# Kernel optimization log

Measured on AMD Instinct MI355X. Metric: run time of the kernel, lower is better.

## Reference

```python
import jax, jax.numpy as jnp
import numpy as np

B, S, H, NH, HD = 2, 2048, 2048, 16, 128
MASK_VALUE = -1e10


def setup_inputs() -> dict:
    key = jax.random.key(0)
    ks = jax.random.split(key, 5)
    scale = 1.0 / np.sqrt(H)
    x = jax.random.normal(ks[0], (B, S, H), dtype=jnp.float32)
    Wq = jax.random.normal(ks[1], (H, NH * HD), dtype=jnp.float32) * scale
    Wk = jax.random.normal(ks[2], (H, NH * HD), dtype=jnp.float32) * scale
    Wv = jax.random.normal(ks[3], (H, NH * HD), dtype=jnp.float32) * scale
    Wo = jax.random.normal(ks[4], (NH * HD, H), dtype=jnp.float32) * scale
    # causal boolean mask (B, S, S) as in decoder-style gemma usage
    mask = jnp.broadcast_to(jnp.tril(jnp.ones((S, S), dtype=bool)), (B, S, S))
    return {"x": x, "mask": mask, "Wq": Wq, "Wk": Wk, "Wv": Wv, "Wo": Wo}


def reference(x, mask, Wq, Wk, Wv, Wo):
    b, s, h = x.shape
    # bias-free QKV projections, split into heads -> (b, nh, s, hd)
    def split_heads(y):
        return y.reshape(b, s, NH, HD).transpose(0, 2, 1, 3)
    q = split_heads(x @ Wq)
    k = split_heads(x @ Wk)
    v = split_heads(x @ Wv)
    scores = jnp.einsum('bhtd,bhTd->bhtT', q, k) / jnp.sqrt(jnp.asarray(HD, x.dtype))
    scores = jnp.where(mask[:, None, :, :], scores, MASK_VALUE)
    weights = jax.nn.softmax(scores, axis=-1)
    out = jnp.einsum('bhtT,bhTd->bhtd', weights, v)
    out = out.transpose(0, 2, 1, 3).reshape(b, s, NH * HD)
    return out @ Wo
```

## Files before the change

kernel.cpp:

```cpp
#include <hip/hip_runtime.h>
#include <hip/hip_bf16.h>
#include <stdint.h>

#define DEVFN __device__ __forceinline__

typedef __attribute__((ext_vector_type(8))) short short8;
typedef __attribute__((ext_vector_type(4))) float f32x4;
typedef __attribute__((ext_vector_type(16))) float f32x16;

constexpr int S_LEN = 2048;
constexpr int HDIM  = 2048;
constexpr int NHEAD = 16;
constexpr int HD    = 128;

DEVFN unsigned short f2bf(float f){
  union { float f; unsigned u; } x; x.f = f;
  unsigned r = x.u + 0x7fffu + ((x.u >> 16) & 1u);
  return (unsigned short)(r >> 16);
}

typedef const __attribute__((address_space(1))) void* gas1_ptr;
typedef __attribute__((address_space(3))) void* las3_ptr;

DEVFN void gl_lds16(const void* g, void* l){
  __builtin_amdgcn_global_load_lds((gas1_ptr)g, (las3_ptr)l, 16, 0, 0);
}

DEVFN f32x4 mfma16(short8 a, short8 b, f32x4 c){
  return __builtin_amdgcn_mfma_f32_16x16x32_bf16(a, b, c, 0, 0, 0);
}

DEVFN f32x16 mfma32(short8 a, short8 b, f32x16 c){
  return __builtin_amdgcn_mfma_f32_32x32x16_bf16(a, b, c, 0, 0, 0);
}

DEVFN unsigned cvtpk_bf16(float lo, float hi){
  unsigned w;
  asm("v_cvt_pk_bf16_f32 %0, %1, %2" : "=v"(w) : "v"(lo), "v"(hi));
  return w;
}


__global__ void cast_x_kernel(const float* __restrict__ in, unsigned short* __restrict__ out){
  int i = (blockIdx.x * 256 + threadIdx.x) * 4;
  float4 v = *(const float4*)(in + i);
  ushort4 o;
  o.x = f2bf(v.x); o.y = f2bf(v.y); o.z = f2bf(v.z); o.w = f2bf(v.w);
  *(ushort4*)(out + i) = o;
}

__global__ void transpose_cast_w(const float* __restrict__ in, unsigned short* __restrict__ out){
  __shared__ float tile[32][33];
  int tx = threadIdx.x, ty = threadIdx.y;
  int kb = blockIdx.x * 32, nb = blockIdx.y * 32;
  #pragma unroll
  for (int i = 0; i < 4; i++)
    tile[ty + i*8][tx] = in[(size_t)(kb + ty + i*8) * HDIM + nb + tx];
  __syncthreads();
  #pragma unroll
  for (int i = 0; i < 4; i++)
    out[(size_t)(nb + ty + i*8) * HDIM + kb + tx] = f2bf(tile[tx][ty + i*8]);
}

__global__ void transpose_v_kernel(const unsigned short* __restrict__ in,
                                   unsigned short* __restrict__ out){
  __shared__ unsigned short tile[32][34];
  int tx = threadIdx.x, ty = threadIdx.y;
  int sb = blockIdx.x * 32, db = blockIdx.y * 32, bh = blockIdx.z;
  const unsigned short* ip = in + (size_t)bh * S_LEN * HD;
  unsigned short* op = out + (size_t)bh * S_LEN * HD;
  #pragma unroll
  for (int i = 0; i < 4; i++)
    tile[ty + i*8][tx] = ip[(size_t)(sb + ty + i*8) * HD + db + tx];
  __syncthreads();
  #pragma unroll
  for (int i = 0; i < 4; i++)
    op[(size_t)(db + ty + i*8) * S_LEN + sb + tx] = tile[tx][ty + i*8];
}


DEVFN void gemm_core_bt(const unsigned short* __restrict__ A,
                        const unsigned short* __restrict__ Bt,
                        int K, int m0, int n0,
                        unsigned short* lsA, unsigned short* lsB,
                        f32x4 (&acc)[4][4]){
  const int t = threadIdx.x;
  const int wid = t >> 6, lane = t & 63;
  const int wr = wid >> 1, wc = wid & 1;
  const int l15 = lane & 15, lg = lane >> 4;

  for (int k0 = 0; k0 < K; k0 += 64){
    __syncthreads();
    #pragma unroll
    for (int i = 0; i < 4; i++){
      int o = (t + i*256) * 16;
      int row = o >> 7;
      int col = (o & 127) ^ ((row & 7) << 4);
      gl_lds16((const char*)A + ((size_t)(m0 + row) * K + k0) * 2 + col, (char*)lsA + o);
    }
    #pragma unroll
    for (int i = 0; i < 4; i++){
      int o = (t + i*256) * 16;
      int row = o >> 7;
      int col = (o & 127) ^ ((row & 7) << 4);
      gl_lds16((const char*)Bt + ((size_t)(n0 + row) * K + k0) * 2 + col, (char*)lsB + o);
    }
    __syncthreads();
    #pragma unroll
    for (int kk = 0; kk < 2; kk++){
      short8 af[4], bfr[4];
      #pragma unroll
      for (int i = 0; i < 4; i++){
        int ra = wr*64 + i*16 + l15;
        af[i]  = *(const short8*)((const char*)lsA + ra*128 + ((kk*64 + lg*16) ^ ((ra & 7) << 4)));
        int rb = wc*64 + i*16 + l15;
        bfr[i] = *(const short8*)((const char*)lsB + rb*128 + ((kk*64 + lg*16) ^ ((rb & 7) << 4)));
      }
      #pragma unroll
      for (int i = 0; i < 4; i++)
        #pragma unroll
        for (int j = 0; j < 4; j++)
          acc[i][j] = mfma16(af[i], bfr[j], acc[i][j]);
    }
  }
}

__global__ __launch_bounds__(256, 2)
void gemm_qkv(const unsigned short* __restrict__ xb, const unsigned short* __restrict__ Wt,
              unsigned short* __restrict__ Qb, unsigned short* __restrict__ Kb,
              unsigned short* __restrict__ Vb){
  __shared__ __align__(16) unsigned short lsA[128*64];
  __shared__ __align__(16) unsigned short lsB[128*64];
  f32x4 acc[4][4];
  const f32x4 z4 = {0.f, 0.f, 0.f, 0.f};
  #pragma unroll
  for (int i = 0; i < 4; i++)
    #pragma unroll
    for (int j = 0; j < 4; j++) acc[i][j] = z4;

  gemm_core_bt(xb, Wt, HDIM, blockIdx.x*128, blockIdx.y*128, lsA, lsB, acc);

  const float qscale = 0.08838834764831845f * 1.4426950408889634f;
  const int t = threadIdx.x, wid = t >> 6, lane = t & 63;
  const int wr = wid >> 1, wc = wid & 1, l15 = lane & 15, lg = lane >> 4;
  #pragma unroll
  for (int j = 0; j < 4; j++){
    int n = blockIdx.y*128 + wc*64 + j*16 + l15;
    int sel = n >> 11, hh = (n >> 7) & 15, d = n & 127;
    unsigned short* base = (sel == 0) ? Qb : ((sel == 1) ? Kb : Vb);
    float sc = (sel == 0) ? qscale : 1.0f;
    #pragma unroll
    for (int i = 0; i < 4; i++){
      #pragma unroll
      for (int r = 0; r < 4; r++){
        int m = blockIdx.x*128 + wr*64 + i*16 + lg*4 + r;
        int bb = m >> 11, ss = m & 2047;
        base[(((size_t)bb * NHEAD + hh) * S_LEN + ss) * HD + d] = f2bf(acc[i][j][r] * sc);
      }
    }
  }
}

__global__ __launch_bounds__(256, 2)
void gemm_out(const unsigned short* __restrict__ Ob, const unsigned short* __restrict__ Wot,
              float* __restrict__ out){
  __shared__ __align__(16) unsigned short lsA[128*64];
  __shared__ __align__(16) unsigned short lsB[128*64];
  f32x4 acc[4][4];
  const f32x4 z4 = {0.f, 0.f, 0.f, 0.f};
  #pragma unroll
  for (int i = 0; i < 4; i++)
    #pragma unroll
    for (int j = 0; j < 4; j++) acc[i][j] = z4;

  gemm_core_bt(Ob, Wot, HDIM, blockIdx.x*128, blockIdx.y*128, lsA, lsB, acc);

  const int t = threadIdx.x, wid = t >> 6, lane = t & 63;
  const int wr = wid >> 1, wc = wid & 1, l15 = lane & 15, lg = lane >> 4;
  #pragma unroll
  for (int i = 0; i < 4; i++){
    #pragma unroll
    for (int r = 0; r < 4; r++){
      int m = blockIdx.x*128 + wr*64 + i*16 + lg*4 + r;
      #pragma unroll
      for (int j = 0; j < 4; j++){
        int n = blockIdx.y*128 + wc*64 + j*16 + l15;
        out[(size_t)m * HDIM + n] = acc[i][j][r];
      }
    }
  }
}

__global__ __launch_bounds__(256, 2)
void attn_kernel(const unsigned short* __restrict__ Q,
                 const unsigned short* __restrict__ Kg,
                 const unsigned short* __restrict__ Vt,
                 unsigned short* __restrict__ Ob){
  __shared__ __align__(16) unsigned short Kl[2][64*128];
  __shared__ __align__(16) unsigned short Vl[2][128*64];

  const int t = threadIdx.x;
  const int wid = t >> 6, lane = t & 63;
  const int l31 = lane & 31, hi = lane >> 5;
  const int L = blockIdx.x;
  const int bh = L & 31;
  const int z = L >> 5;
  const int qt = (z < 8) ? z : 23 - z;
  const int b = bh >> 4, h = bh & 15;
  const unsigned short* Qp = Q  + (size_t)bh * S_LEN * HD;
  const unsigned short* Kp = Kg + (size_t)bh * S_LEN * HD;
  const unsigned short* Vp = Vt + (size_t)bh * S_LEN * HD;
  const int q0 = qt * 128;
  const int wrow0 = q0 + wid * 32;
  const int qrow = wrow0 + l31;
  const int nt = 2 * qt + 2;

  auto stage = [&](int buf, int k0){
    #pragma unroll
    for (int i = 0; i < 4; i++){
      int o = (t + i*256) * 16;
      int row = o >> 8;
      int col = (o & 255) ^ ((row & 15) << 4);
      gl_lds16((const char*)(Kp + (size_t)(k0 + row) * HD) + col, (char*)&Kl[buf][0] + o);
    }
    #pragma unroll
    for (int i = 0; i < 4; i++){
      int o = (t + i*256) * 16;
      int row = o >> 7;
      int col = (o & 127) ^ ((row & 7) << 4);
      gl_lds16((const char*)(Vp + (size_t)row * S_LEN + k0) + col, (char*)&Vl[buf][0] + o);
    }
  };

  short8 qf[8];
  #pragma unroll
  for (int dk = 0; dk < 8; dk++)
    qf[dk] = *(const short8*)(Qp + (size_t)qrow * HD + dk*16 + hi*8);

  f32x16 oacc[4];
  #pragma unroll
  for (int db = 0; db < 4; db++)
    #pragma unroll
    for (int r = 0; r < 16; r++) oacc[db][r] = 0.f;
  float mrun = -1e30f, lsum = 0.f;

  stage(0, 0);
  asm volatile("s_waitcnt vmcnt(0)" ::: "memory");
  __builtin_amdgcn_s_barrier();

  int cur = 0;
  #pragma unroll 1
  for (int tdx = 0; tdx < nt; tdx++){
    if (tdx + 1 < nt) stage(cur ^ 1, (tdx + 1) * 64);
    const int k0 = tdx * 64;

    if (k0 <= wrow0 + 31){
      const char* Kb_ = (const char*)&Kl[cur][0];
      const char* Vb_ = (const char*)&Vl[cur][0];

      f32x16 sacc[2];
      #pragma unroll
      for (int cb = 0; cb < 2; cb++)
        #pragma unroll
        for (int r = 0; r < 16; r++) sacc[cb][r] = 0.f;
      __builtin_amdgcn_s_setprio(1);
      #pragma unroll
      for (int dk = 0; dk < 8; dk++){
        #pragma unroll
        for (int cb = 0; cb < 2; cb++){
          int kr = cb*32 + l31;
          short8 af = *(const short8*)(Kb_ + kr*256 + ((dk*32 + hi*16) ^ ((kr & 15) << 4)));
          sacc[cb] = mfma32(af, qf[dk], sacc[cb]);
        }
      }
      __builtin_amdgcn_s_setprio(0);

      if (k0 + 64 > wrow0){
        #pragma unroll
        for (int cb = 0; cb < 2; cb++)
          #pragma unroll
          for (int r = 0; r < 16; r++){
            int kcol = k0 + cb*32 + (r & 3) + 8*(r >> 2) + 4*hi;
            if (kcol > qrow) sacc[cb][r] = -1e30f;
          }
      }

      float mv[8];
      #pragma unroll
      for (int i = 0; i < 8; i++)
        mv[i] = fmaxf(fmaxf(sacc[0][i], sacc[0][i+8]), fmaxf(sacc[1][i], sacc[1][i+8]));
      #pragma unroll
      for (int s = 4; s > 0; s >>= 1)
        #pragma unroll
        for (int i = 0; i < 4; i++)
          if (i < s) mv[i] = fmaxf(mv[i], mv[i+s]);
      float mx = fmaxf(mv[0], __shfl_xor(mv[0], 32, 64));
      if (!__all(mx <= mrun + 8.f)){
        float mnew = fmaxf(mrun, mx);
        float alpha = exp2f(mrun - mnew);
        mrun = mnew;
        lsum *= alpha;
        #pragma unroll
        for (int db = 0; db < 4; db++)
          #pragma unroll
          for (int r = 0; r < 16; r++) oacc[db][r] *= alpha;
      }
      float ls = 0.f;
      #pragma unroll
      for (int cb = 0; cb < 2; cb++)
        #pragma unroll
        for (int r = 0; r < 16; r++){
          float p = exp2f(sacc[cb][r] - mrun);
          sacc[cb][r] = p;
          ls += p;
        }
      lsum += ls;

      short8 pa[4];
      #pragma unroll
      for (int ks = 0; ks < 4; ks++){
        int cb = ks >> 1, bs = (ks & 1) * 8;
        unsigned A1 = cvtpk_bf16(sacc[cb][bs+4], sacc[cb][bs+5]);
        unsigned B1 = cvtpk_bf16(sacc[cb][bs+0], sacc[cb][bs+1]);
        unsigned A2 = cvtpk_bf16(sacc[cb][bs+6], sacc[cb][bs+7]);
        unsigned B2 = cvtpk_bf16(sacc[cb][bs+2], sacc[cb][bs+3]);
        unsigned oA1 = __shfl_xor(A1, 32, 64), oB1 = __shfl_xor(B1, 32, 64);
        unsigned oA2 = __shfl_xor(A2, 32, 64), oB2 = __shfl_xor(B2, 32, 64);
        union { unsigned u[4]; short8 v; } pk;
        pk.u[0] = hi ? oA1 : B1;
        pk.u[1] = hi ? oA2 : B2;
        pk.u[2] = hi ? A1 : oB1;
        pk.u[3] = hi ? A2 : oB2;
        pa[ks] = pk.v;
      }

      __builtin_amdgcn_s_setprio(1);
      #pragma unroll
      for (int ks = 0; ks < 4; ks++){
        #pragma unroll
        for (int db = 0; db < 4; db++){
          int vr = db*32 + l31;
          short8 vf = *(const short8*)(Vb_ + vr*128 + ((ks*32 + hi*16) ^ ((vr & 7) << 4)));
          oacc[db] = mfma32(vf, pa[ks], oacc[db]);
        }
      }
      __builtin_amdgcn_s_setprio(0);
    }

    asm volatile("s_waitcnt vmcnt(0)" ::: "memory");
    __builtin_amdgcn_s_barrier();
    cur ^= 1;
  }

  float lt = lsum + __shfl_xor(lsum, 32, 64);
  float inv = 1.f / lt;
  #pragma unroll
  for (int db = 0; db < 4; db++)
    #pragma unroll
    for (int r = 0; r < 16; r++) oacc[db][r] *= inv;

  char* reg_lds = (char*)&Kl[0][0] + wid * 8192;
  #pragma unroll
  for (int ms = 0; ms < 8; ms++){
    int db = ms >> 1, bs = (ms & 1) * 8;
    unsigned A1 = cvtpk_bf16(oacc[db][bs+4], oacc[db][bs+5]);
    unsigned B1 = cvtpk_bf16(oacc[db][bs+0], oacc[db][bs+1]);
    unsigned A2 = cvtpk_bf16(oacc[db][bs+6], oacc[db][bs+7]);
    unsigned B2 = cvtpk_bf16(oacc[db][bs+2], oacc[db][bs+3]);
    unsigned oA1 = __shfl_xor(A1, 32, 64), oB1 = __shfl_xor(B1, 32, 64);
    unsigned oA2 = __shfl_xor(A2, 32, 64), oB2 = __shfl_xor(B2, 32, 64);
    union { unsigned u[4]; short8 v; } pk;
    pk.u[0] = hi ? oA1 : B1;
    pk.u[1] = hi ? oA2 : B2;
    pk.u[2] = hi ? A1 : oB1;
    pk.u[3] = hi ? A2 : oB2;
    int byteo = l31*256 + ((ms*32 + hi*16) ^ ((l31 & 7) << 4));
    *(short8*)(reg_lds + byteo) = pk.v;
  }
  #pragma unroll
  for (int i = 0; i < 8; i++){
    int r = (lane >> 4) + i*4;
    int c = lane & 15;
    short8 v = *(const short8*)(reg_lds + r*256 + ((c*16) ^ ((r & 7) << 4)));
    *(short8*)(Ob + ((size_t)(b * S_LEN + wrow0 + r)) * 2048 + h*128 + c*8) = v;
  }
}

extern "C" void kernel_launch(void* const* d_in, const int* in_sizes, int n_in,
                              void* d_out, int out_size, void* d_ws, size_t ws_size,
                              hipStream_t stream){
  const float* x  = (const float*)d_in[0];
  const float* Wq = (const float*)d_in[2];
  const float* Wk = (const float*)d_in[3];
  const float* Wv = (const float*)d_in[4];
  const float* Wo = (const float*)d_in[5];

  char* ws = (char*)d_ws;
  unsigned short* xb  = (unsigned short*)(ws);
  unsigned short* Wt  = (unsigned short*)(ws + 16777216);
  unsigned short* Wot = (unsigned short*)(ws + 41943040);
  unsigned short* Qb  = (unsigned short*)(ws + 50331648);
  unsigned short* Kb  = (unsigned short*)(ws + 67108864);
  unsigned short* Vb  = (unsigned short*)(ws + 83886080);
  unsigned short* Vt  = Wt;
  unsigned short* Ob  = xb;

  dim3 tb(32, 8);
  cast_x_kernel<<<8192, 256, 0, stream>>>(x, xb);
  transpose_cast_w<<<dim3(64, 64), tb, 0, stream>>>(Wq, Wt);
  transpose_cast_w<<<dim3(64, 64), tb, 0, stream>>>(Wk, Wt + 2048*2048);
  transpose_cast_w<<<dim3(64, 64), tb, 0, stream>>>(Wv, Wt + 2*2048*2048);
  transpose_cast_w<<<dim3(64, 64), tb, 0, stream>>>(Wo, Wot);

  gemm_qkv<<<dim3(32, 48), 256, 0, stream>>>(xb, Wt, Qb, Kb, Vb);

  transpose_v_kernel<<<dim3(64, 4, 32), tb, 0, stream>>>(Vb, Vt);

  attn_kernel<<<512, 256, 0, stream>>>(Qb, Kb, Vt, Ob);

  gemm_out<<<dim3(32, 16), 256, 0, stream>>>(Ob, Wot, (float*)d_out);
}
```

Before: 257.4 us.

## Triple-buffer GEMM LDS with 256x128 tiles, swizzled grid, fused weight casts

Both GEMMs are rewritten around a shared core. It uses 512-thread blocks with 256x128 output tiles and a three-stage LDS ring fed by async global-to-LDS loads. Partial `s_waitcnt vmcnt` waits plus a single barrier per k-step let the next two tiles load while the current one computes. A block-index swizzle groups neighbouring tiles for L2 reuse, and the four weight transpose-casts become one launch over a z dimension. The cost is about 144KB of LDS per block, which allows only one block per CU, and this relies on latency hiding coming from the pipeline rather than from occupancy.

Measured after the change: 261.8 us. About the same (+1.7%).

```diff
diff --git a/kernel.cpp b/kernel.cpp
--- a/kernel.cpp
+++ b/kernel.cpp
@@ -49,17 +49,21 @@
   *(ushort4*)(out + i) = o;
 }
 
-__global__ void transpose_cast_w(const float* __restrict__ in, unsigned short* __restrict__ out){
+__global__ void transpose_cast_w4(const float* __restrict__ w0, const float* __restrict__ w1,
+                                  const float* __restrict__ w2, const float* __restrict__ w3,
+                                  unsigned short* __restrict__ out){
   __shared__ float tile[32][33];
   int tx = threadIdx.x, ty = threadIdx.y;
-  int kb = blockIdx.x * 32, nb = blockIdx.y * 32;
+  int kb = blockIdx.x * 32, nb = blockIdx.y * 32, z = blockIdx.z;
+  const float* in = (z == 0) ? w0 : (z == 1) ? w1 : (z == 2) ? w2 : w3;
+  unsigned short* op = out + (size_t)z * HDIM * HDIM;
   #pragma unroll
   for (int i = 0; i < 4; i++)
     tile[ty + i*8][tx] = in[(size_t)(kb + ty + i*8) * HDIM + nb + tx];
   __syncthreads();
   #pragma unroll
   for (int i = 0; i < 4; i++)
-    out[(size_t)(nb + ty + i*8) * HDIM + kb + tx] = f2bf(tile[tx][ty + i*8]);
+    op[(size_t)(nb + ty + i*8) * HDIM + kb + tx] = f2bf(tile[tx][ty + i*8]);
 }
 
 __global__ void transpose_v_kernel(const unsigned short* __restrict__ in,
@@ -78,43 +82,55 @@
     op[(size_t)(db + ty + i*8) * S_LEN + sb + tx] = tile[tx][ty + i*8];
 }
 
-
-DEVFN void gemm_core_bt(const unsigned short* __restrict__ A,
-                        const unsigned short* __restrict__ Bt,
-                        int K, int m0, int n0,
-                        unsigned short* lsA, unsigned short* lsB,
-                        f32x4 (&acc)[4][4]){
-  const int t = threadIdx.x;
-  const int wid = t >> 6, lane = t & 63;
+DEVFN void gemm_core3(const unsigned short* __restrict__ A,
+                      const unsigned short* __restrict__ Bt,
+                      int K, int m0, int n0, char* ls, f32x4 (&acc)[4][4]){
+  const int tid = threadIdx.x;
+  const int wid = tid >> 6, lane = tid & 63;
   const int wr = wid >> 1, wc = wid & 1;
   const int l15 = lane & 15, lg = lane >> 4;
-
-  for (int k0 = 0; k0 < K; k0 += 64){
-    __syncthreads();
+  const int nt = K >> 6;
+
+  auto stage = [&](int buf, int kt){
+    const char* Ab = (const char*)A + (size_t)kt * 128;
+    const char* Bb = (const char*)Bt + (size_t)kt * 128;
+    char* lb = ls + buf * 49152;
     #pragma unroll
     for (int i = 0; i < 4; i++){
-      int o = (t + i*256) * 16;
+      int o = (tid + i*512) * 16;
       int row = o >> 7;
       int col = (o & 127) ^ ((row & 7) << 4);
-      gl_lds16((const char*)A + ((size_t)(m0 + row) * K + k0) * 2 + col, (char*)lsA + o);
-    }
-    #pragma unroll
-    for (int i = 0; i < 4; i++){
-      int o = (t + i*256) * 16;
-      int row = o >> 7;
-      int col = (o & 127) ^ ((row & 7) << 4);
-      gl_lds16((const char*)Bt + ((size_t)(n0 + row) * K + k0) * 2 + col, (char*)lsB + o);
-    }
-    __syncthreads();
+      gl_lds16(Ab + (size_t)(m0 + row) * (K*2) + col, lb + o);
+    }
+    #pragma unroll
+    for (int i = 4; i < 6; i++){
+      int o = (tid + i*512) * 16;
+      int ob = o - 32768;
+      int row = ob >> 7;
+      int col = (ob & 127) ^ ((row & 7) << 4);
+      gl_lds16(Bb + (size_t)(n0 + row) * (K*2) + col, lb + o);
+    }
+  };
+
+  stage(0, 0);
+  stage(1, 1);
+  #pragma unroll 1
+  for (int kt = 0; kt < nt; kt++){
+    if (kt + 1 < nt) asm volatile("s_waitcnt vmcnt(6)" ::: "memory");
+    else             asm volatile("s_waitcnt vmcnt(0)" ::: "memory");
+    __builtin_amdgcn_s_barrier();
+    if (kt + 2 < nt) stage((kt + 2) % 3, kt + 2);
+
+    const char* lb = ls + (kt % 3) * 49152;
     #pragma unroll
     for (int kk = 0; kk < 2; kk++){
       short8 af[4], bfr[4];
       #pragma unroll
       for (int i = 0; i < 4; i++){
         int ra = wr*64 + i*16 + l15;
-        af[i]  = *(const short8*)((const char*)lsA + ra*128 + ((kk*64 + lg*16) ^ ((ra & 7) << 4)));
+        af[i]  = *(const short8*)(lb + ra*128 + ((kk*64 + lg*16) ^ ((ra & 7) << 4)));
         int rb = wc*64 + i*16 + l15;
-        bfr[i] = *(const short8*)((const char*)lsB + rb*128 + ((kk*64 + lg*16) ^ ((rb & 7) << 4)));
+        bfr[i] = *(const short8*)(lb + 32768 + rb*128 + ((kk*64 + lg*16) ^ ((rb & 7) << 4)));
       }
       #pragma unroll
       for (int i = 0; i < 4; i++)
@@ -125,12 +141,11 @@
   }
 }
 
-__global__ __launch_bounds__(256, 2)
+__global__ __launch_bounds__(512, 2)
 void gemm_qkv(const unsigned short* __restrict__ xb, const unsigned short* __restrict__ Wt,
               unsigned short* __restrict__ Qb, unsigned short* __restrict__ Kb,
               unsigned short* __restrict__ Vb){
-  __shared__ __align__(16) unsigned short lsA[128*64];
-  __shared__ __align__(16) unsigned short lsB[128*64];
+  __shared__ __align__(16) char ls[147456];
   f32x4 acc[4][4];
   const f32x4 z4 = {0.f, 0.f, 0.f, 0.f};
   #pragma unroll
@@ -138,14 +153,18 @@
     #pragma unroll
     for (int j = 0; j < 4; j++) acc[i][j] = z4;
 
-  gemm_core_bt(xb, Wt, HDIM, blockIdx.x*128, blockIdx.y*128, lsA, lsB, acc);
+  int swz = (blockIdx.x & 7) * 96 + (blockIdx.x >> 3);
+  int m0 = (swz / 48) * 256;
+  int n0 = (swz % 48) * 128;
+
+  gemm_core3(xb, Wt, HDIM, m0, n0, ls, acc);
 
   const float qscale = 0.08838834764831845f * 1.4426950408889634f;
-  const int t = threadIdx.x, wid = t >> 6, lane = t & 63;
+  const int tid = threadIdx.x, wid = tid >> 6, lane = tid & 63;
   const int wr = wid >> 1, wc = wid & 1, l15 = lane & 15, lg = lane >> 4;
   #pragma unroll
   for (int j = 0; j < 4; j++){
-    int n = blockIdx.y*128 + wc*64 + j*16 + l15;
+    int n = n0 + wc*64 + j*16 + l15;
     int sel = n >> 11, hh = (n >> 7) & 15, d = n & 127;
     unsigned short* base = (sel == 0) ? Qb : ((sel == 1) ? Kb : Vb);
     float sc = (sel == 0) ? qscale : 1.0f;
@@ -153,7 +172,7 @@
     for (int i = 0; i < 4; i++){
       #pragma unroll
       for (int r = 0; r < 4; r++){
-        int m = blockIdx.x*128 + wr*64 + i*16 + lg*4 + r;
+        int m = m0 + wr*64 + i*16 + lg*4 + r;
         int bb = m >> 11, ss = m & 2047;
         base[(((size_t)bb * NHEAD + hh) * S_LEN + ss) * HD + d] = f2bf(acc[i][j][r] * sc);
       }
@@ -161,11 +180,10 @@
   }
 }
 
-__global__ __launch_bounds__(256, 2)
+__global__ __launch_bounds__(512, 2)
 void gemm_out(const unsigned short* __restrict__ Ob, const unsigned short* __restrict__ Wot,
               float* __restrict__ out){
-  __shared__ __align__(16) unsigned short lsA[128*64];
-  __shared__ __align__(16) unsigned short lsB[128*64];
+  __shared__ __align__(16) char ls[147456];
   f32x4 acc[4][4];
   const f32x4 z4 = {0.f, 0.f, 0.f, 0.f};
   #pragma unroll
@@ -173,18 +191,22 @@
     #pragma unroll
     for (int j = 0; j < 4; j++) acc[i][j] = z4;
 
-  gemm_core_bt(Ob, Wot, HDIM, blockIdx.x*128, blockIdx.y*128, lsA, lsB, acc);
-
-  const int t = threadIdx.x, wid = t >> 6, lane = t & 63;
+  int swz = (blockIdx.x & 7) * 32 + (blockIdx.x >> 3);
+  int m0 = (swz / 16) * 256;
+  int n0 = (swz % 16) * 128;
+
+  gemm_core3(Ob, Wot, HDIM, m0, n0, ls, acc);
+
+  const int tid = threadIdx.x, wid = tid >> 6, lane = tid & 63;
   const int wr = wid >> 1, wc = wid & 1, l15 = lane & 15, lg = lane >> 4;
   #pragma unroll
   for (int i = 0; i < 4; i++){
     #pragma unroll
     for (int r = 0; r < 4; r++){
-      int m = blockIdx.x*128 + wr*64 + i*16 + lg*4 + r;
+      int m = m0 + wr*64 + i*16 + lg*4 + r;
       #pragma unroll
       for (int j = 0; j < 4; j++){
-        int n = blockIdx.y*128 + wc*64 + j*16 + l15;
+        int n = n0 + wc*64 + j*16 + l15;
         out[(size_t)m * HDIM + n] = acc[i][j][r];
       }
     }
@@ -407,16 +429,13 @@
 
   dim3 tb(32, 8);
   cast_x_kernel<<<8192, 256, 0, stream>>>(x, xb);
-  transpose_cast_w<<<dim3(64, 64), tb, 0, stream>>>(Wq, Wt);
-  transpose_cast_w<<<dim3(64, 64), tb, 0, stream>>>(Wk, Wt + 2048*2048);
-  transpose_cast_w<<<dim3(64, 64), tb, 0, stream>>>(Wv, Wt + 2*2048*2048);
-  transpose_cast_w<<<dim3(64, 64), tb, 0, stream>>>(Wo, Wot);
-
-  gemm_qkv<<<dim3(32, 48), 256, 0, stream>>>(xb, Wt, Qb, Kb, Vb);
+  transpose_cast_w4<<<dim3(64, 64, 4), tb, 0, stream>>>(Wq, Wk, Wv, Wo, Wt);
+
+  gemm_qkv<<<768, 512, 0, stream>>>(xb, Wt, Qb, Kb, Vb);
 
   transpose_v_kernel<<<dim3(64, 4, 32), tb, 0, stream>>>(Vb, Vt);
 
   attn_kernel<<<512, 256, 0, stream>>>(Qb, Kb, Vt, Ob);
 
-  gemm_out<<<dim3(32, 16), 256, 0, stream>>>(Ob, Wot, (float*)d_out);
-}
+  gemm_out<<<256, 512, 0, stream>>>(Ob, Wot, (float*)d_out);
+}
```

## Fuse V transpose into QKV GEMM epilogue and batch weight transposes

Applied to the files above, without the earlier changes.

The QKV GEMM epilogue now writes V directly in transposed (d-major) layout by staging the bf16 tile through swizzled LDS and doing vectorized stores. This removes the separate V transpose kernel and its extra global read and write. The four weight transpose-cast launches are merged into one 3D-grid launch. Launch bounds are raised to target four blocks per CU, which risks register pressure.

New measurement: 242.7 us. -5.7%, faster.

```diff
diff --git a/kernel.cpp b/kernel.cpp
--- a/kernel.cpp
+++ b/kernel.cpp
@@ -49,45 +49,33 @@
   *(ushort4*)(out + i) = o;
 }
 
-__global__ void transpose_cast_w(const float* __restrict__ in, unsigned short* __restrict__ out){
+__global__ void transpose_cast_w4(const float* __restrict__ w0, const float* __restrict__ w1,
+                                  const float* __restrict__ w2, const float* __restrict__ w3,
+                                  unsigned short* __restrict__ out){
   __shared__ float tile[32][33];
   int tx = threadIdx.x, ty = threadIdx.y;
-  int kb = blockIdx.x * 32, nb = blockIdx.y * 32;
+  int kb = blockIdx.x * 32, nb = blockIdx.y * 32, z = blockIdx.z;
+  const float* in = (z == 0) ? w0 : (z == 1) ? w1 : (z == 2) ? w2 : w3;
+  unsigned short* op = out + (size_t)z * HDIM * HDIM;
   #pragma unroll
   for (int i = 0; i < 4; i++)
     tile[ty + i*8][tx] = in[(size_t)(kb + ty + i*8) * HDIM + nb + tx];
   __syncthreads();
   #pragma unroll
   for (int i = 0; i < 4; i++)
-    out[(size_t)(nb + ty + i*8) * HDIM + kb + tx] = f2bf(tile[tx][ty + i*8]);
-}
-
-__global__ void transpose_v_kernel(const unsigned short* __restrict__ in,
-                                   unsigned short* __restrict__ out){
-  __shared__ unsigned short tile[32][34];
-  int tx = threadIdx.x, ty = threadIdx.y;
-  int sb = blockIdx.x * 32, db = blockIdx.y * 32, bh = blockIdx.z;
-  const unsigned short* ip = in + (size_t)bh * S_LEN * HD;
-  unsigned short* op = out + (size_t)bh * S_LEN * HD;
-  #pragma unroll
-  for (int i = 0; i < 4; i++)
-    tile[ty + i*8][tx] = ip[(size_t)(sb + ty + i*8) * HD + db + tx];
-  __syncthreads();
-  #pragma unroll
-  for (int i = 0; i < 4; i++)
-    op[(size_t)(db + ty + i*8) * S_LEN + sb + tx] = tile[tx][ty + i*8];
+    op[(size_t)(nb + ty + i*8) * HDIM + kb + tx] = f2bf(tile[tx][ty + i*8]);
 }
 
 
 DEVFN void gemm_core_bt(const unsigned short* __restrict__ A,
                         const unsigned short* __restrict__ Bt,
-                        int K, int m0, int n0,
-                        unsigned short* lsA, unsigned short* lsB,
-                        f32x4 (&acc)[4][4]){
+                        int K, int m0, int n0, char* ls, f32x4 (&acc)[4][4]){
   const int t = threadIdx.x;
   const int wid = t >> 6, lane = t & 63;
   const int wr = wid >> 1, wc = wid & 1;
   const int l15 = lane & 15, lg = lane >> 4;
+  char* lsA = ls;
+  char* lsB = ls + 16384;
 
   for (int k0 = 0; k0 < K; k0 += 64){
     __syncthreads();
@@ -96,14 +84,14 @@
       int o = (t + i*256) * 16;
       int row = o >> 7;
       int col = (o & 127) ^ ((row & 7) << 4);
-      gl_lds16((const char*)A + ((size_t)(m0 + row) * K + k0) * 2 + col, (char*)lsA + o);
+      gl_lds16((const char*)A + ((size_t)(m0 + row) * K + k0) * 2 + col, lsA + o);
     }
     #pragma unroll
     for (int i = 0; i < 4; i++){
       int o = (t + i*256) * 16;
       int row = o >> 7;
       int col = (o & 127) ^ ((row & 7) << 4);
-      gl_lds16((const char*)Bt + ((size_t)(n0 + row) * K + k0) * 2 + col, (char*)lsB + o);
+      gl_lds16((const char*)Bt + ((size_t)(n0 + row) * K + k0) * 2 + col, lsB + o);
     }
     __syncthreads();
     #pragma unroll
@@ -112,9 +100,9 @@
       #pragma unroll
       for (int i = 0; i < 4; i++){
         int ra = wr*64 + i*16 + l15;
-        af[i]  = *(const short8*)((const char*)lsA + ra*128 + ((kk*64 + lg*16) ^ ((ra & 7) << 4)));
+        af[i]  = *(const short8*)(lsA + ra*128 + ((kk*64 + lg*16) ^ ((ra & 7) << 4)));
         int rb = wc*64 + i*16 + l15;
-        bfr[i] = *(const short8*)((const char*)lsB + rb*128 + ((kk*64 + lg*16) ^ ((rb & 7) << 4)));
+        bfr[i] = *(const short8*)(lsB + rb*128 + ((kk*64 + lg*16) ^ ((rb & 7) << 4)));
       }
       #pragma unroll
       for (int i = 0; i < 4; i++)
@@ -125,12 +113,11 @@
   }
 }
 
-__global__ __launch_bounds__(256, 2)
+__global__ __launch_bounds__(256, 4)
 void gemm_qkv(const unsigned short* __restrict__ xb, const unsigned short* __restrict__ Wt,
               unsigned short* __restrict__ Qb, unsigned short* __restrict__ Kb,
-              unsigned short* __restrict__ Vb){
-  __shared__ __align__(16) unsigned short lsA[128*64];
-  __shared__ __align__(16) unsigned short lsB[128*64];
+              unsigned short* __restrict__ Vt){
+  __shared__ __align__(16) char ls[32768];
   f32x4 acc[4][4];
   const f32x4 z4 = {0.f, 0.f, 0.f, 0.f};
   #pragma unroll
@@ -138,34 +125,65 @@
     #pragma unroll
     for (int j = 0; j < 4; j++) acc[i][j] = z4;
 
-  gemm_core_bt(xb, Wt, HDIM, blockIdx.x*128, blockIdx.y*128, lsA, lsB, acc);
+  const int m0 = blockIdx.x * 128;
+  const int n0 = blockIdx.y * 128;
+  gemm_core_bt(xb, Wt, HDIM, m0, n0, ls, acc);
 
   const float qscale = 0.08838834764831845f * 1.4426950408889634f;
   const int t = threadIdx.x, wid = t >> 6, lane = t & 63;
   const int wr = wid >> 1, wc = wid & 1, l15 = lane & 15, lg = lane >> 4;
-  #pragma unroll
-  for (int j = 0; j < 4; j++){
-    int n = blockIdx.y*128 + wc*64 + j*16 + l15;
-    int sel = n >> 11, hh = (n >> 7) & 15, d = n & 127;
-    unsigned short* base = (sel == 0) ? Qb : ((sel == 1) ? Kb : Vb);
-    float sc = (sel == 0) ? qscale : 1.0f;
-    #pragma unroll
-    for (int i = 0; i < 4; i++){
-      #pragma unroll
-      for (int r = 0; r < 4; r++){
-        int m = blockIdx.x*128 + wr*64 + i*16 + lg*4 + r;
-        int bb = m >> 11, ss = m & 2047;
-        base[(((size_t)bb * NHEAD + hh) * S_LEN + ss) * HD + d] = f2bf(acc[i][j][r] * sc);
-      }
-    }
-  }
-}
-
-__global__ __launch_bounds__(256, 2)
+  const int bb = m0 >> 11, ss0 = m0 & 2047;
+
+  if (n0 < 4096){
+    unsigned short* base = (n0 < 2048) ? Qb : Kb;
+    const float sc = (n0 < 2048) ? qscale : 1.0f;
+    #pragma unroll
+    for (int j = 0; j < 4; j++){
+      int n = n0 + wc*64 + j*16 + l15;
+      int hh = (n >> 7) & 15, d = n & 127;
+      #pragma unroll
+      for (int i = 0; i < 4; i++){
+        #pragma unroll
+        for (int r = 0; r < 4; r++){
+          int ss = ss0 + wr*64 + i*16 + lg*4 + r;
+          base[(((size_t)bb * NHEAD + hh) * S_LEN + ss) * HD + d] = f2bf(acc[i][j][r] * sc);
+        }
+      }
+    }
+  } else {
+    const int hh = (n0 - 4096) >> 7;
+    __syncthreads();
+    #pragma unroll
+    for (int j = 0; j < 4; j++){
+      int nn = wc*64 + j*16 + l15;
+      int rowb = nn*256 + (((nn & 7) << 4));
+      #pragma unroll
+      for (int i = 0; i < 4; i++){
+        int mmb = (wr*64 + i*16 + lg*4) * 2;
+        unsigned w0 = cvtpk_bf16(acc[i][j][0], acc[i][j][1]);
+        unsigned w1 = cvtpk_bf16(acc[i][j][2], acc[i][j][3]);
+        *(unsigned*)(ls + nn*256 + ((mmb    ) ^ ((nn & 7) << 4))) = w0;
+        *(unsigned*)(ls + nn*256 + ((mmb + 4) ^ ((nn & 7) << 4))) = w1;
+      }
+      (void)rowb;
+    }
+    __syncthreads();
+    unsigned short* vout = Vt + (((size_t)bb * NHEAD + hh) * HD) * S_LEN;
+    #pragma unroll
+    for (int p = 0; p < 8; p++){
+      int idx = p*256 + t;
+      int d = idx >> 4;
+      int m8 = (idx & 15) * 8;
+      short8 v = *(const short8*)(ls + d*256 + ((m8*2) ^ ((d & 7) << 4)));
+      *(short8*)(vout + (size_t)d * S_LEN + ss0 + m8) = v;
+    }
+  }
+}
+
+__global__ __launch_bounds__(256, 4)
 void gemm_out(const unsigned short* __restrict__ Ob, const unsigned short* __restrict__ Wot,
               float* __restrict__ out){
-  __shared__ __align__(16) unsigned short lsA[128*64];
-  __shared__ __align__(16) unsigned short lsB[128*64];
+  __shared__ __align__(16) char ls[32768];
   f32x4 acc[4][4];
   const f32x4 z4 = {0.f, 0.f, 0.f, 0.f};
   #pragma unroll
@@ -173,7 +191,9 @@
     #pragma unroll
     for (int j = 0; j < 4; j++) acc[i][j] = z4;
 
-  gemm_core_bt(Ob, Wot, HDIM, blockIdx.x*128, blockIdx.y*128, lsA, lsB, acc);
+  const int m0 = blockIdx.x * 128;
+  const int n0 = blockIdx.y * 128;
+  gemm_core_bt(Ob, Wot, HDIM, m0, n0, ls, acc);
 
   const int t = threadIdx.x, wid = t >> 6, lane = t & 63;
   const int wr = wid >> 1, wc = wid & 1, l15 = lane & 15, lg = lane >> 4;
@@ -181,10 +201,10 @@
   for (int i = 0; i < 4; i++){
     #pragma unroll
     for (int r = 0; r < 4; r++){
-      int m = blockIdx.x*128 + wr*64 + i*16 + lg*4 + r;
+      int m = m0 + wr*64 + i*16 + lg*4 + r;
       #pragma unroll
       for (int j = 0; j < 4; j++){
-        int n = blockIdx.y*128 + wc*64 + j*16 + l15;
+        int n = n0 + wc*64 + j*16 + l15;
         out[(size_t)m * HDIM + n] = acc[i][j][r];
       }
     }
@@ -401,20 +421,14 @@
   unsigned short* Wot = (unsigned short*)(ws + 41943040);
   unsigned short* Qb  = (unsigned short*)(ws + 50331648);
   unsigned short* Kb  = (unsigned short*)(ws + 67108864);
-  unsigned short* Vb  = (unsigned short*)(ws + 83886080);
-  unsigned short* Vt  = Wt;
+  unsigned short* Vt  = (unsigned short*)(ws + 83886080);
   unsigned short* Ob  = xb;
 
   dim3 tb(32, 8);
   cast_x_kernel<<<8192, 256, 0, stream>>>(x, xb);
-  transpose_cast_w<<<dim3(64, 64), tb, 0, stream>>>(Wq, Wt);
-  transpose_cast_w<<<dim3(64, 64), tb, 0, stream>>>(Wk, Wt + 2048*2048);
-  transpose_cast_w<<<dim3(64, 64), tb, 0, stream>>>(Wv, Wt + 2*2048*2048);
-  transpose_cast_w<<<dim3(64, 64), tb, 0, stream>>>(Wo, Wot);
-
-  gemm_qkv<<<dim3(32, 48), 256, 0, stream>>>(xb, Wt, Qb, Kb, Vb);
-
-  transpose_v_kernel<<<dim3(64, 4, 32), tb, 0, stream>>>(Vb, Vt);
+  transpose_cast_w4<<<dim3(64, 64, 4), tb, 0, stream>>>(Wq, Wk, Wv, Wo, Wt);
+
+  gemm_qkv<<<dim3(32, 48), 256, 0, stream>>>(xb, Wt, Qb, Kb, Vt);
 
   attn_kernel<<<512, 256, 0, stream>>>(Qb, Kb, Vt, Ob);
 
```
